# Kernel optimization log

Hardware: AMD Instinct MI355X
Metric: run time of the kernel (lower is better)

Reference implementation:

```python
import jax, jax.numpy as jnp
import numpy as np

B, S, T = 64, 48, 48
E, H = 512, 1024
V_SRC, V_TGT = 32000, 32000
PAD = 0


def setup_inputs() -> dict:
    key = jax.random.key(0)
    ks = jax.random.split(key, 24)
    def g(k, shape, scale=0.05):
        return jax.random.normal(k, shape, dtype=jnp.float32) * scale
    return {
        "src_ids": jax.random.randint(ks[0], (S, B), 0, V_SRC),
        "tgt_ids": jax.random.randint(ks[1], (T, B), 0, V_TGT),
        "src_lengths": S,
        "src_emb": g(ks[2], (V_SRC, E)).at[PAD].set(0.0),
        "tgt_emb": g(ks[3], (V_TGT, E)).at[PAD].set(0.0),
        "cnn_w": g(ks[4], (E, E, 2)),
        "cnn_b": g(ks[5], (E,)),
        "enc_Wih_f": g(ks[6], (4 * H, E)),
        "enc_Whh_f": g(ks[7], (4 * H, H)),
        "enc_bih_f": g(ks[8], (4 * H,)),
        "enc_bhh_f": g(ks[9], (4 * H,)),
        "enc_Wih_b": g(ks[10], (4 * H, E)),
        "enc_Whh_b": g(ks[11], (4 * H, H)),
        "enc_bih_b": g(ks[12], (4 * H,)),
        "enc_bhh_b": g(ks[13], (4 * H,)),
        "dec_Wih": g(ks[14], (4 * H, E + H)),
        "dec_Whh": g(ks[15], (4 * H, H)),
        "dec_bih": g(ks[16], (4 * H,)),
        "dec_bhh": g(ks[17], (4 * H,)),
        "Wh": g(ks[18], (H, 2 * H)),
        "Wc": g(ks[19], (H, 2 * H)),
        "Watt": g(ks[20], (H, 2 * H)),
        "Wcomb": g(ks[21], (H, 3 * H)),
        "Wvocab": g(ks[22], (V_TGT, H)),
    }


def _lstm_cell(x, h, c, Wih, Whh, bih, bhh):
    gates = x @ Wih.T + h @ Whh.T + bih + bhh  # (b, 4h)
    i, f, g, o = jnp.split(gates, 4, axis=-1)
    c_new = jax.nn.sigmoid(f) * c + jax.nn.sigmoid(i) * jnp.tanh(g)
    h_new = jax.nn.sigmoid(o) * jnp.tanh(c_new)
    return h_new, c_new


def _forward(src_ids, tgt_ids,
             src_emb, tgt_emb, cnn_w, cnn_b,
             enc_Wih_f, enc_Whh_f, enc_bih_f, enc_bhh_f,
             enc_Wih_b, enc_Whh_b, enc_bih_b, enc_bhh_b,
             dec_Wih, dec_Whh, dec_bih, dec_bhh,
             Wh, Wc, Watt, Wcomb, Wvocab):
    b = src_ids.shape[1]
    h = Wh.shape[0]
    # ---- encode ----
    X = src_emb[src_ids]                       # (S, b, E)
    Xc = jnp.transpose(X, (1, 2, 0))           # (b, E, S)
    # Conv1d kernel_size=2, padding='same' in torch pads (left=0, right=1)
    Xc = jax.lax.conv_general_dilated(Xc, cnn_w, window_strides=(1,),
                                      padding=[(0, 1)],
                                      dimension_numbers=("NCH", "OIH", "NCH"))
    Xc = Xc + cnn_b[None, :, None]
    X = jnp.transpose(Xc, (2, 0, 1))           # (S, b, E)

    h0 = jnp.zeros((b, h), dtype=X.dtype)
    def fstep(carry, x_t):
        hh, cc = carry
        hh, cc = _lstm_cell(x_t, hh, cc, enc_Wih_f, enc_Whh_f, enc_bih_f, enc_bhh_f)
        return (hh, cc), hh
    def bstep(carry, x_t):
        hh, cc = carry
        hh, cc = _lstm_cell(x_t, hh, cc, enc_Wih_b, enc_Whh_b, enc_bih_b, enc_bhh_b)
        return (hh, cc), hh
    (hf, cf), out_f = jax.lax.scan(fstep, (h0, h0), X)
    (hb, cb), out_b = jax.lax.scan(bstep, (h0, h0), X[::-1])
    out_b = out_b[::-1]
    enc_hiddens = jnp.concatenate([out_f, out_b], axis=-1)   # (S, b, 2h)
    enc_hiddens = jnp.transpose(enc_hiddens, (1, 0, 2))      # (b, S, 2h)
    dec_h = jnp.concatenate([hf, hb], axis=1) @ Wh.T         # (b, h)
    dec_c = jnp.concatenate([cf, cb], axis=1) @ Wc.T         # (b, h)

    # ---- decode ----
    enc_proj = enc_hiddens @ Watt.T            # (b, S, h)
    enc_mask = jnp.zeros((b, enc_hiddens.shape[1]), dtype=bool)  # all full length
    Y = tgt_emb[tgt_ids[:-1]]                  # (T-1, b, E)

    def dstep(carry, Y_t):
        hh, cc, o_prev = carry
        ybar = jnp.concatenate([o_prev, Y_t], axis=1)        # (b, h+E)
        hh, cc = _lstm_cell(ybar, hh, cc, dec_Wih, dec_Whh, dec_bih, dec_bhh)
        e_t = jnp.einsum("bh,bsh->bs", hh, enc_proj)
        e_t = jnp.where(enc_mask, -jnp.inf, e_t)
        alpha = jax.nn.softmax(e_t, axis=-1)
        a_t = jnp.einsum("bs,bsd->bd", alpha, enc_hiddens)   # (b, 2h)
        O_t = jnp.tanh(jnp.concatenate([a_t, hh], axis=1) @ Wcomb.T)  # dropout rate 0
        return (hh, cc, O_t), O_t

    o0 = jnp.zeros((b, h), dtype=X.dtype)
    _, combined = jax.lax.scan(dstep, (dec_h, dec_c, o0), Y)  # (T-1, b, h)

    P = jax.nn.log_softmax(combined @ Wvocab.T, axis=-1)      # (T-1, b, V)
    gold = tgt_ids[1:]                                        # (T-1, b)
    logp = jnp.take_along_axis(P, gold[..., None], axis=-1)[..., 0]
    tmask = (gold != PAD).astype(P.dtype)
    return (logp * tmask).sum(axis=0)                         # (b,)


def reference(src_ids, tgt_ids, src_lengths,
              src_emb, tgt_emb, cnn_w, cnn_b,
              enc_Wih_f, enc_Whh_f, enc_bih_f, enc_bhh_f,
              enc_Wih_b, enc_Whh_b, enc_bih_b, enc_bhh_b,
              dec_Wih, dec_Whh, dec_bih, dec_bhh,
              Wh, Wc, Watt, Wcomb, Wvocab):
    # src_lengths == S for every sentence (packed seq degenerates to full-length LSTM)
    return _forward(src_ids, tgt_ids, src_emb, tgt_emb, cnn_w, cnn_b,
                    enc_Wih_f, enc_Whh_f, enc_bih_f, enc_bhh_f,
                    enc_Wih_b, enc_Whh_b, enc_bih_b, enc_bhh_b,
                    dec_Wih, dec_Whh, dec_bih, dec_bhh,
                    Wh, Wc, Watt, Wcomb, Wvocab)
```

## Files before the change

kernel.cpp:

```cpp
#include <hip/hip_runtime.h>
#include <hip/hip_bf16.h>
#include <math.h>

using f32x4 = __attribute__((ext_vector_type(4))) float;
using s16x8 = __attribute__((ext_vector_type(8))) short;
typedef unsigned short u16;
typedef unsigned int u32;
typedef unsigned long long u64;

#define MFMA16(a,b,c) __builtin_amdgcn_mfma_f32_16x16x32_bf16(a,b,c,0,0,0)
#define SCOPE_A __HIP_MEMORY_SCOPE_AGENT
#define FP 16

__device__ __forceinline__ float bf2f(u16 u){
  union { u32 i; float f; } v; v.i = ((u32)u) << 16; return v.f;
}
__device__ __forceinline__ u16 f2bf(float f){
  union { float f; u32 i; } v; v.f = f;
  u32 x = v.i;
  return (u16)((x + 0x7fffu + ((x >> 16) & 1u)) >> 16);
}
__device__ __forceinline__ float sigm(float x){ return 1.0f/(1.0f + expf(-x)); }

__device__ __forceinline__ s16x8 pack8(const float* p){
  s16x8 r;
  #pragma unroll
  for (int i = 0; i < 8; ++i) r[i] = (short)f2bf(p[i]);
  return r;
}

__device__ __forceinline__ void coh_st32(void* p, u32 v){
  __hip_atomic_store((u32*)p, v, __ATOMIC_RELAXED, SCOPE_A);
}
__device__ __forceinline__ float u2f(u32 u){ union { u32 i; float f; } v; v.i = u; return v.f; }
__device__ __forceinline__ u32 f2u(float f){ union { float f; u32 i; } v; v.f = f; return v.i; }

__device__ __forceinline__ void poll(const int* flags, int n, int gen){
  for (int i = threadIdx.x; i < n; i += 256)
    while (__hip_atomic_load(flags + i*FP, __ATOMIC_RELAXED, SCOPE_A) < gen)
      __builtin_amdgcn_s_sleep(1);
  __syncthreads();
}
__device__ __forceinline__ void setflag(int* flag, int gen){
  __syncthreads();
  if (threadIdx.x == 0)
    __hip_atomic_store(flag, gen, __ATOMIC_RELAXED, SCOPE_A);
}

__device__ __forceinline__ void gemm_k1024(
    const u16* ap, const char* wb0, const char* wb1, int xo, int addb,
    f32x4& a0, f32x4& a1)
{
  #pragma unroll
  for (int c = 0; c < 2; ++c){
    s16x8 st[16];
    #pragma unroll
    for (int q = 0; q < 16; ++q) st[q] = *(const s16x8*)(ap + c*512 + q*32);
    #pragma unroll
    for (int q = 0; q < 16; ++q){
      int cb = (addb + (c*512 + q*32)*2) ^ xo;
      a0 = MFMA16(st[q], *(const s16x8*)(wb0 + cb), a0);
      a1 = MFMA16(st[q], *(const s16x8*)(wb1 + cb), a1);
    }
  }
}

__global__ void k_zero(float* __restrict__ p, long n){
  long i = (long)blockIdx.x*blockDim.x + threadIdx.x;
  long st = (long)gridDim.x*blockDim.x;
  for (; i < n; i += st) p[i] = 0.0f;
}

__global__ void k_cast_bf16(const float* __restrict__ src, u16* __restrict__ dst, long n){
  long i = ((long)blockIdx.x*blockDim.x + threadIdx.x)*4;
  long st = (long)gridDim.x*blockDim.x*4;
  for (; i < n; i += st){
    float4 v = *(const float4*)(src + i);
    *(ushort4*)(dst + i) = make_ushort4(f2bf(v.x), f2bf(v.y), f2bf(v.z), f2bf(v.w));
  }
}

__global__ void k_addv(const float* __restrict__ a, const float* __restrict__ b,
                       float* __restrict__ d, int n){
  int i = blockIdx.x*blockDim.x + threadIdx.x;
  if (i < n) d[i] = a[i] + b[i];
}

__global__ void k_repack_conv(const float* __restrict__ w, u16* __restrict__ dst){
  int i = blockIdx.x*256 + threadIdx.x;
  int o = i >> 9, ii = i & 511;
  dst[(size_t)o*1024 + ii]       = f2bf(w[((size_t)o*512 + ii)*2 + 0]);
  dst[(size_t)o*1024 + 512 + ii] = f2bf(w[((size_t)o*512 + ii)*2 + 1]);
}

__global__ void k_build_wy(const float* __restrict__ dWih, u16* __restrict__ Wy){
  int i = blockIdx.x*256 + threadIdx.x;
  int r = i >> 9, c = i & 511;
  Wy[(size_t)r*512 + c] = f2bf(dWih[(size_t)r*1536 + 1024 + c]);
}

__global__ void k_split_wcomb(const float* __restrict__ Wcomb,
                              u16* __restrict__ Wca, u16* __restrict__ Whp){
  int r = blockIdx.x;
  for (int c = threadIdx.x; c < 2048; c += 256)
    Wca[(size_t)r*2048 + c] = f2bf(Wcomb[(size_t)r*3072 + c]);
  for (int c = threadIdx.x; c < 1024; c += 256)
    Whp[(size_t)r*1024 + c] = f2bf(Wcomb[(size_t)r*3072 + 2048 + c]);
}

__global__ void k_gather_src(const int* __restrict__ ids, const float* __restrict__ emb,
                             u16* __restrict__ Aconv){
  int s = blockIdx.x;
  int b = blockIdx.y;
  int e = threadIdx.x*4;
  float4 v = make_float4(0.f,0.f,0.f,0.f);
  if (s < 48){ int id = ids[s*64 + b]; v = *(const float4*)(emb + (size_t)id*512 + e); }
  ushort4 u = make_ushort4(f2bf(v.x), f2bf(v.y), f2bf(v.z), f2bf(v.w));
  if (s < 48) *(ushort4*)(Aconv + ((size_t)(s*64 + b))*1024 + e) = u;
  if (s >= 1) *(ushort4*)(Aconv + ((size_t)((s-1)*64 + b))*1024 + 512 + e) = u;
}

__global__ void k_gather_y(const int* __restrict__ ids, const float* __restrict__ emb,
                           u16* __restrict__ Y){
  int t = blockIdx.x; int b = blockIdx.y; int e = threadIdx.x*4;
  int id = ids[t*64 + b];
  float4 v = *(const float4*)(emb + (size_t)id*512 + e);
  *(ushort4*)(Y + ((size_t)(t*64 + b))*512 + e) = make_ushort4(f2bf(v.x), f2bf(v.y), f2bf(v.z), f2bf(v.w));
}

template<bool OUT_BF16, bool PACKG>
__global__ __launch_bounds__(256) void k_gemm(
    const u16* __restrict__ A0, long lda0,
    const u16* __restrict__ A1, long lda1, int ksplit,
    const u16* __restrict__ W, int K,
    void* __restrict__ Out, long ldc,
    const float* __restrict__ bias)
{
  __shared__ __align__(16) u16 As[64][72];
  __shared__ __align__(16) u16 Ws[64][72];
  const int t = threadIdx.x;
  const int m0 = blockIdx.x*64, n0 = blockIdx.y*64;
  const int w = t >> 6, l = t & 63, lr = l & 15, lh = l >> 4;
  const int sr = t >> 2, sk = (t & 3) << 4;

  f32x4 acc[4] = {{0,0,0,0},{0,0,0,0},{0,0,0,0},{0,0,0,0}};

  for (int kc = 0; kc < K; kc += 64){
    {
      const u16* wp = W + (size_t)(n0 + sr)*K + kc + sk;
      *(s16x8*)&Ws[sr][sk]     = *(const s16x8*)wp;
      *(s16x8*)&Ws[sr][sk + 8] = *(const s16x8*)(wp + 8);
    }
    {
      const u16* ap = (kc < ksplit)
        ? A0 + (size_t)(m0 + sr)*lda0 + kc
        : A1 + (size_t)(m0 + sr)*lda1 + (kc - ksplit);
      ap += sk;
      *(s16x8*)&As[sr][sk]     = *(const s16x8*)ap;
      *(s16x8*)&As[sr][sk + 8] = *(const s16x8*)(ap + 8);
    }
    __syncthreads();
    #pragma unroll
    for (int kk = 0; kk < 64; kk += 32){
      s16x8 a = *(const s16x8*)&As[w*16 + lr][kk + lh*8];
      #pragma unroll
      for (int ct = 0; ct < 4; ++ct){
        s16x8 bfr = *(const s16x8*)&Ws[ct*16 + lr][kk + lh*8];
        acc[ct] = MFMA16(a, bfr, acc[ct]);
      }
    }
    __syncthreads();
  }
  #pragma unroll
  for (int ct = 0; ct < 4; ++ct){
    #pragma unroll
    for (int rr = 0; rr < 4; ++rr){
      long row = m0 + w*16 + lh*4 + rr;
      long col = n0 + ct*16 + lr;
      float v = acc[ct][rr];
      if (bias) v += bias[col];
      if (PACKG){
        long time = row >> 6, b = row & 63, g = col >> 10, j = col & 1023;
        ((u16*)Out)[((time*1024 + j)*4 + g)*64 + b] = f2bf(v);
      } else {
        long oi = row*ldc + col;
        if (OUT_BF16) ((u16*)Out)[oi] = f2bf(v);
        else          ((float*)Out)[oi] = v;
      }
    }
  }
}

__global__ __launch_bounds__(256) void k_enc_persist(
    const float* __restrict__ WhhF, const float* __restrict__ WhhB,
    const u16* __restrict__ GfP, const u16* __restrict__ GbP,
    u16* __restrict__ hEF, u16* __restrict__ hEB,
    const u16* __restrict__ hzero,
    float* __restrict__ cF, float* __restrict__ cB,
    u16* __restrict__ Aatt, u16* __restrict__ cfbf, u16* __restrict__ cbbf,
    int* Eflags)
{
  extern __shared__ char smem[];
  const int t = threadIdx.x, blk = blockIdx.x;
  const int dir = blk >> 6;
  const int j0 = (blk & 63) << 4;
  const float* Wsrc = dir ? WhhB : WhhF;
  const u16* GP = dir ? GbP : GfP;
  float* c = dir ? cB : cF;
  u16* cobf = dir ? cbbf : cfbf;
  u16* hE = dir ? hEB : hEF;

  for (int q = t; q < 64*128; q += 256){
    int row = q >> 7;
    int ck = (q & 127) << 3;
    int wrow = ((row >> 4)*1024) + j0 + (row & 15);
    s16x8 pk = pack8(Wsrc + (size_t)wrow*1024 + ck);
    *(s16x8*)(smem + row*2048 + ((ck*2) ^ ((row & 7) << 4))) = pk;
  }
  __syncthreads();

  const int w = t >> 6, l = t & 63, lr = l & 15, lh = l >> 4;
  const int lane_m = w*16 + lr;
  const int koff = lh*8;
  const char* wp0 = smem + lr*2048;
  const char* wp1 = smem + (16 + lr)*2048;
  const char* wp2 = smem + (32 + lr)*2048;
  const char* wp3 = smem + (48 + lr)*2048;
  const int xo = (lr & 7) << 4;
  const int j = j0 + lr;
  int* myflags = Eflags + dir*64*FP;
  const int myidx = blk & 63;

  for (int s = 0; s < 48; ++s){
    const u16* hin = s ? (hE + (size_t)(s - 1)*65536) : hzero;
    u16* hout      = hE + (size_t)s*65536;
    const int time = dir ? 47 - s : s;
    if (s) poll(myflags, 64, s);
    f32x4 a0 = {0,0,0,0}, a1 = {0,0,0,0}, a2 = {0,0,0,0}, a3 = {0,0,0,0};
    const u16* ap = hin + (size_t)lane_m*1024 + koff;
    #pragma unroll
    for (int cc = 0; cc < 2; ++cc){
      s16x8 st[16];
      #pragma unroll
      for (int q = 0; q < 16; ++q) st[q] = *(const s16x8*)(ap + cc*512 + q*32);
      #pragma unroll
      for (int q = 0; q < 16; ++q){
        int cb = ((cc*512 + q*32 + koff)*2) ^ xo;
        a0 = MFMA16(st[q], *(const s16x8*)(wp0 + cb), a0);
        a1 = MFMA16(st[q], *(const s16x8*)(wp1 + cb), a1);
        a2 = MFMA16(st[q], *(const s16x8*)(wp2 + cb), a2);
        a3 = MFMA16(st[q], *(const s16x8*)(wp3 + cb), a3);
      }
    }
    #pragma unroll
    for (int rr = 0; rr < 4; ++rr){
      int b = w*16 + lh*4 + rr;
      const u16* gp = GP + (((size_t)time*1024 + j)*4)*64 + b;
      float gi = a0[rr] + bf2f(gp[0]);
      float gf = a1[rr] + bf2f(gp[64]);
      float gg = a2[rr] + bf2f(gp[128]);
      float go = a3[rr] + bf2f(gp[192]);
      float cn = sigm(gf)*c[b*1024 + j] + sigm(gi)*tanhf(gg);
      float hn = sigm(go)*tanhf(cn);
      c[b*1024 + j] = cn;
      u16 hb = f2bf(hn);
      u32 hi2 = __shfl_down((u32)hb, 1);
      if ((lr & 1) == 0)
        coh_st32((u32*)hout + ((b*1024 + j) >> 1), (u32)hb | (hi2 << 16));
      Aatt[((size_t)b*48 + time)*2048 + dir*1024 + j] = hb;
      if (s == 47) cobf[b*1024 + j] = f2bf(cn);
    }
    setflag(myflags + myidx*FP, s + 1);
  }
}

__global__ __launch_bounds__(256) void k_dec_persist(
    const float* __restrict__ dWih, const float* __restrict__ dWhh,
    const u16* __restrict__ GyP,
    const u16* __restrict__ encP, const u16* __restrict__ encWc,
    const u16* __restrict__ Whp,
    const u16* __restrict__ hbinit, u16* __restrict__ hD,
    float* __restrict__ cdec,
    float* __restrict__ hp, u16* __restrict__ Cbf,
    const u16* __restrict__ obf_zero,
    int* Gflags, int* G2flags, int* Cflags)
{
  extern __shared__ char smem[];
  const int t = threadIdx.x, blk = blockIdx.x;
  const int w = t >> 6, l = t & 63, lr = l & 15, lh = l >> 4;
  const int lane_m = w*16 + lr;
  const int koff = lh*8;
  const int xo = (lr & 7) << 4;

  if (blk < 128){
    const int j0 = blk << 3;
    for (int q = t; q < 32*256; q += 256){
      int row = q >> 8;
      int ck = (q & 255) << 3;
      int wrow = ((row >> 3)*1024) + j0 + (row & 7);
      const float* src = (ck < 1024) ? dWih + (size_t)wrow*1536 + ck
                                     : dWhh + (size_t)wrow*1024 + (ck - 1024);
      s16x8 pk = pack8(src);
      *(s16x8*)(smem + row*4096 + ((ck*2) ^ ((row & 7) << 4))) = pk;
    }
    char* WhpL = smem + 131072;
    for (int q = t; q < 8*128; q += 256){
      int row = q >> 7, ck = (q & 127) << 3;
      s16x8 v = *(const s16x8*)(Whp + (size_t)(j0 + row)*1024 + ck);
      *(s16x8*)(WhpL + row*2048 + ((ck*2) ^ ((row & 7) << 4))) = v;
    }
    __syncthreads();
    const char* wp0 = smem + lr*4096;
    const char* wp1 = smem + (16 + lr)*4096;
    const char* wph = WhpL + (lr & 7)*2048;
    const int jj = lr & 7, gsel = lr >> 3;
    const int j = j0 + jj;

    s16x8 hreg[32];
    {
      const u16* ap = hbinit + (size_t)lane_m*1024 + koff;
      #pragma unroll
      for (int q = 0; q < 32; ++q) hreg[q] = *(const s16x8*)(ap + q*32);
    }

    for (int tt = 0; tt < 47; ++tt){
      u16* hout = hD + (size_t)tt*65536;
      f32x4 a0 = {0,0,0,0}, a1 = {0,0,0,0};
      #pragma unroll
      for (int q = 0; q < 32; ++q){
        int cb = ((1024 + q*32 + koff)*2) ^ xo;
        a0 = MFMA16(hreg[q], *(const s16x8*)(wp0 + cb), a0);
        a1 = MFMA16(hreg[q], *(const s16x8*)(wp1 + cb), a1);
      }
      if (tt) poll(Cflags, 64, tt);
      const u16* Ao = tt ? (Cbf + (size_t)(tt - 1)*65536) : obf_zero;
      gemm_k1024(Ao + (size_t)lane_m*1024 + koff, wp0, wp1, xo, koff*2, a0, a1);
      #pragma unroll
      for (int rr = 0; rr < 4; ++rr){
        float v0 = a0[rr], v1 = a1[rr];
        float p0 = __shfl_xor(v0, 8, 64);
        float p1 = __shfl_xor(v1, 8, 64);
        if (gsel == 0){
          int b = w*16 + lh*4 + rr;
          const u16* gp = GyP + (((size_t)tt*1024 + j)*4)*64 + b;
          float gi = v0 + bf2f(gp[0]);
          float gf = p0 + bf2f(gp[64]);
          float gg = v1 + bf2f(gp[128]);
          float go = p1 + bf2f(gp[192]);
          float cn = sigm(gf)*cdec[b*1024 + j] + sigm(gi)*tanhf(gg);
          float hn = sigm(go)*tanhf(cn);
          cdec[b*1024 + j] = cn;
          u16 hb = f2bf(hn);
          u32 hi2 = __shfl_down((u32)hb, 1);
          if ((jj & 1) == 0)
            coh_st32((u32*)hout + ((b*1024 + j) >> 1), (u32)hb | (hi2 << 16));
        }
      }
      setflag(Gflags + blk*FP, tt + 1);
      poll(Gflags, 128, tt + 1);
      {
        const u16* ap = hout + (size_t)lane_m*1024 + koff;
        #pragma unroll
        for (int q = 0; q < 32; ++q) hreg[q] = *(const s16x8*)(ap + q*32);
      }
      f32x4 hpacc = {0,0,0,0};
      #pragma unroll
      for (int q = 0; q < 32; ++q){
        int cb = ((q*32 + koff)*2) ^ xo;
        s16x8 bw = {0,0,0,0,0,0,0,0};
        if (lr < 8) bw = *(const s16x8*)(wph + cb);
        hpacc = MFMA16(hreg[q], bw, hpacc);
      }
      if (lr < 8){
        float* hpout = hp + (size_t)tt*65536;
        #pragma unroll
        for (int rr = 0; rr < 4; ++rr)
          coh_st32(&hpout[(size_t)(w*16 + lh*4 + rr)*1024 + j0 + lr], f2u(hpacc[rr]));
      }
      setflag(G2flags + blk*FP, tt + 1);
    }
  } else {
    const int b = blk - 128;
    u16* encPL = (u16*)smem;
    float* hs  = (float*)(smem + 98304);
    float* es  = (float*)(smem + 102400);
    float* al  = es + 48;
    float* sred= al + 48;
    for (int q = t; q < 48*128; q += 256){
      int row = q >> 7, ck = (q & 127) << 3;
      *(s16x8*)&encPL[row*1024 + ck] =
        *(const s16x8*)(encP + ((size_t)b*48 + row)*1024 + ck);
    }
    __syncthreads();

    for (int tt = 0; tt < 47; ++tt){
      poll(Gflags, 128, tt + 1);
      const u16* hrow = hD + (size_t)tt*65536 + (size_t)b*1024;
      {
        ushort4 v4 = ((const ushort4*)hrow)[t];
        hs[4*t]     = bf2f(v4.x);
        hs[4*t + 1] = bf2f(v4.y);
        hs[4*t + 2] = bf2f(v4.z);
        hs[4*t + 3] = bf2f(v4.w);
      }
      __syncthreads();
      for (int s2 = w; s2 < 48; s2 += 4){
        float p = 0.f;
        #pragma unroll
        for (int i = 0; i < 16; ++i)
          p += hs[l + 64*i]*bf2f(encPL[s2*1024 + l + 64*i]);
        #pragma unroll
        for (int d = 32; d >= 1; d >>= 1) p += __shfl_xor(p, d, 64);
        if (l == 0) es[s2] = p;
      }
      __syncthreads();
      if (t == 0){
        float m = es[0];
        for (int s2 = 1; s2 < 48; ++s2) m = fmaxf(m, es[s2]);
        float su = 0.f;
        for (int s2 = 0; s2 < 48; ++s2) su += expf(es[s2] - m);
        sred[0] = m; sred[1] = 1.0f/su;
      }
      __syncthreads();
      if (t < 48) al[t] = expf(es[t] - sred[0])*sred[1];
      __syncthreads();
      poll(G2flags, 128, tt + 1);
      int c0 = t*4;
      float4 hpv = *(const float4*)(hp + (size_t)tt*65536 + (size_t)b*1024 + c0);
      float acc0 = 0.f, acc1 = 0.f, acc2 = 0.f, acc3 = 0.f;
      const u16* ew = encWc + (size_t)b*48*1024 + c0;
      #pragma unroll 4
      for (int s2 = 0; s2 < 48; ++s2){
        float wgt = al[s2];
        ushort4 e4 = *(const ushort4*)(ew + (size_t)s2*1024);
        acc0 += wgt*bf2f(e4.x); acc1 += wgt*bf2f(e4.y);
        acc2 += wgt*bf2f(e4.z); acc3 += wgt*bf2f(e4.w);
      }
      float v0 = tanhf(hpv.x + acc0), v1 = tanhf(hpv.y + acc1);
      float v2 = tanhf(hpv.z + acc2), v3 = tanhf(hpv.w + acc3);
      size_t oi = (size_t)tt*65536 + (size_t)b*1024 + c0;
      coh_st32((u32*)Cbf + (oi >> 1),     (u32)f2bf(v0) | ((u32)f2bf(v1) << 16));
      coh_st32((u32*)Cbf + (oi >> 1) + 1, (u32)f2bf(v2) | ((u32)f2bf(v3) << 16));
      setflag(Cflags + b*FP, tt + 1);
    }
  }
}

#define VNS 25
__global__ __launch_bounds__(256) void k_vocab_lse(
    const u16* __restrict__ Cbf, const u16* __restrict__ Wv, float2* __restrict__ partials)
{
  __shared__ __align__(16) u16 As[128][72];
  __shared__ __align__(16) u16 Bs[128][72];
  __shared__ float2 mg[128][2];
  int rb = blockIdx.x, sp = blockIdx.y;
  int m0 = rb*128;
  int t = threadIdx.x, w = t >> 6, l = t & 63, lr = l & 15, lh = l >> 4;
  int wr = w >> 1, wc = w & 1;
  int sr = t >> 1, sk = (t & 1) << 5;

  float mrun[4][4], srun[4][4];
  #pragma unroll
  for (int m = 0; m < 4; ++m)
    #pragma unroll
    for (int rr = 0; rr < 4; ++rr){ mrun[m][rr] = -INFINITY; srun[m][rr] = 0.f; }

  for (int nt = 0; nt < 10; ++nt){
    int n0 = sp*1280 + nt*128;
    f32x4 acc[4][4];
    #pragma unroll
    for (int m = 0; m < 4; ++m)
      #pragma unroll
      for (int n = 0; n < 4; ++n) acc[m][n] = (f32x4){0,0,0,0};

    for (int kc = 0; kc < 1024; kc += 64){
      int ar = m0 + sr; if (ar > 3007) ar = 3007;
      const u16* ap = Cbf + (size_t)ar*1024 + kc + sk;
      const u16* wp = Wv + (size_t)(n0 + sr)*1024 + kc + sk;
      #pragma unroll
      for (int q = 0; q < 4; ++q){
        *(s16x8*)&As[sr][sk + q*8] = *(const s16x8*)(ap + q*8);
        *(s16x8*)&Bs[sr][sk + q*8] = *(const s16x8*)(wp + q*8);
      }
      __syncthreads();
      #pragma unroll
      for (int kk = 0; kk < 64; kk += 32){
        s16x8 af[4], bf[4];
        #pragma unroll
        for (int m = 0; m < 4; ++m)
          af[m] = *(const s16x8*)&As[wr*64 + m*16 + lr][kk + lh*8];
        #pragma unroll
        for (int n = 0; n < 4; ++n)
          bf[n] = *(const s16x8*)&Bs[wc*64 + n*16 + lr][kk + lh*8];
        #pragma unroll
        for (int m = 0; m < 4; ++m)
          #pragma unroll
          for (int n = 0; n < 4; ++n)
            acc[m][n] = MFMA16(af[m], bf[n], acc[m][n]);
      }
      __syncthreads();
    }
    #pragma unroll
    for (int m = 0; m < 4; ++m){
      #pragma unroll
      for (int rr = 0; rr < 4; ++rr){
        float tm = fmaxf(fmaxf(acc[m][0][rr], acc[m][1][rr]),
                         fmaxf(acc[m][2][rr], acc[m][3][rr]));
        #pragma unroll
        for (int d = 1; d < 16; d <<= 1) tm = fmaxf(tm, __shfl_xor(tm, d, 64));
        float ts = expf(acc[m][0][rr] - tm) + expf(acc[m][1][rr] - tm)
                 + expf(acc[m][2][rr] - tm) + expf(acc[m][3][rr] - tm);
        #pragma unroll
        for (int d = 1; d < 16; d <<= 1) ts += __shfl_xor(ts, d, 64);
        if (tm > mrun[m][rr]){ srun[m][rr] = srun[m][rr]*expf(mrun[m][rr] - tm) + ts; mrun[m][rr] = tm; }
        else srun[m][rr] += ts*expf(tm - mrun[m][rr]);
      }
    }
  }
  __syncthreads();
  if (lr == 0){
    #pragma unroll
    for (int m = 0; m < 4; ++m)
      #pragma unroll
      for (int rr = 0; rr < 4; ++rr)
        mg[wr*64 + m*16 + lh*4 + rr][wc] = make_float2(mrun[m][rr], srun[m][rr]);
  }
  __syncthreads();
  if (t < 128){
    float2 p0 = mg[t][0], p1 = mg[t][1];
    float m = fmaxf(p0.x, p1.x);
    float s = p0.y*expf(p0.x - m) + p1.y*expf(p1.x - m);
    long row = m0 + t;
    if (row < 3008) partials[row*VNS + sp] = make_float2(m, s);
  }
}

__global__ void k_lse(const float2* __restrict__ partials, float* __restrict__ lse){
  int r = blockIdx.x*256 + threadIdx.x;
  if (r >= 3008) return;
  float m = -INFINITY, s = 0.f;
  for (int i = 0; i < VNS; ++i){
    float2 p = partials[r*VNS + i];
    if (p.x > m){ s = s*expf(m - p.x) + p.y; m = p.x; }
    else s += p.y*expf(p.x - m);
  }
  lse[r] = m + logf(s);
}

__global__ __launch_bounds__(256) void k_gold(const u16* __restrict__ Cbf,
                                              const u16* __restrict__ Wv,
                                              const int* __restrict__ tgt,
                                              float* __restrict__ gold){
  int w = threadIdx.x >> 6, l = threadIdx.x & 63;
  int r = blockIdx.x*4 + w;
  int tt = r >> 6, b = r & 63;
  int gid = tgt[(tt + 1)*64 + b];
  const u16* cp = Cbf + (size_t)r*1024;
  const u16* wp = Wv + (size_t)gid*1024;
  float p = 0.f;
  for (int i = l; i < 1024; i += 64) p += bf2f(cp[i])*bf2f(wp[i]);
  for (int d = 32; d >= 1; d >>= 1) p += __shfl_xor(p, d, 64);
  if (l == 0) gold[r] = p;
}

__global__ void k_final(const float* __restrict__ gold, const float* __restrict__ lse,
                        const int* __restrict__ tgt, float* __restrict__ out){
  int b = threadIdx.x;
  if (b >= 64) return;
  float acc = 0.f;
  for (int t = 0; t < 47; ++t){
    int gid = tgt[(t + 1)*64 + b];
    if (gid != 0) acc += gold[t*64 + b] - lse[t*64 + b];
  }
  out[b] = acc;
}

extern "C" void kernel_launch(void* const* d_in, const int* in_sizes, int n_in,
                              void* d_out, int out_size, void* d_ws, size_t ws_size,
                              hipStream_t stream)
{
  (void)in_sizes; (void)n_in; (void)out_size; (void)ws_size;
  const int*   src_ids = (const int*)d_in[0];
  const int*   tgt_ids = (const int*)d_in[1];
  const float* src_emb = (const float*)d_in[3];
  const float* tgt_emb = (const float*)d_in[4];
  const float* cnn_w   = (const float*)d_in[5];
  const float* cnn_b   = (const float*)d_in[6];
  const float* eWih_f  = (const float*)d_in[7];
  const float* eWhh_f  = (const float*)d_in[8];
  const float* ebih_f  = (const float*)d_in[9];
  const float* ebhh_f  = (const float*)d_in[10];
  const float* eWih_b  = (const float*)d_in[11];
  const float* eWhh_b  = (const float*)d_in[12];
  const float* ebih_b  = (const float*)d_in[13];
  const float* ebhh_b  = (const float*)d_in[14];
  const float* dWih    = (const float*)d_in[15];
  const float* dWhh    = (const float*)d_in[16];
  const float* dbih    = (const float*)d_in[17];
  const float* dbhh    = (const float*)d_in[18];
  const float* Wh      = (const float*)d_in[19];
  const float* Wc      = (const float*)d_in[20];
  const float* Watt    = (const float*)d_in[21];
  const float* Wcomb   = (const float*)d_in[22];
  const float* Wvocab  = (const float*)d_in[23];

  char* ws = (char*)d_ws;
  size_t off = 0;
  auto alloc = [&](size_t bytes)->char*{
    char* p = ws + off;
    off = (off + bytes + 255) & ~(size_t)255;
    return p;
  };

  float* cF     = (float*)alloc((size_t)65536*4);
  float* cB     = (float*)alloc((size_t)65536*4);
  u16* obf_zero = (u16*)alloc((size_t)65536*2);
  int* bar      = (int*)alloc(40960);
  size_t zero_floats = ((size_t)262144*2 + 131072 + 40960)/4;
  int* Eflags  = bar;
  int* Gflags  = bar + 2048;
  int* G2flags = bar + 4096;
  int* Cflags  = bar + 6144;

  u16* Wconv_bf = (u16*)alloc((size_t)512*1024*2);
  u16* Wih_f_bf = (u16*)alloc((size_t)4096*512*2);
  u16* Wih_b_bf = (u16*)alloc((size_t)4096*512*2);
  u16* Wy_bf    = (u16*)alloc((size_t)4096*512*2);
  u16* Wh_bf    = (u16*)alloc((size_t)1024*2048*2);
  u16* Wc_bf    = (u16*)alloc((size_t)1024*2048*2);
  u16* Watt_bf  = (u16*)alloc((size_t)1024*2048*2);
  u16* Wca_bf   = (u16*)alloc((size_t)1024*2048*2);
  u16* Whp_bf   = (u16*)alloc((size_t)1024*1024*2);
  u16* Wv_bf    = (u16*)alloc((size_t)32000*1024*2);
  float* benc_f = (float*)alloc(4096*4);
  float* benc_b = (float*)alloc(4096*4);
  float* bdec   = (float*)alloc(4096*4);

  u16* Aconv    = (u16*)alloc((size_t)3072*1024*2);
  u16* Xc       = (u16*)alloc((size_t)3072*512*2);
  u16* GfP      = (u16*)alloc((size_t)48*1024*256*2);
  u16* GbP      = (u16*)alloc((size_t)48*1024*256*2);
  u16* GyP      = (u16*)alloc((size_t)47*1024*256*2);
  u16* Ybf      = (u16*)alloc((size_t)3008*512*2);
  u16* Aatt     = (u16*)alloc((size_t)3072*2048*2);
  u16* encP     = (u16*)alloc((size_t)3072*1024*2);
  u16* encWc    = (u16*)alloc((size_t)3072*1024*2);
  u16* hEF      = (u16*)alloc((size_t)48*65536*2);
  u16* hEB      = (u16*)alloc((size_t)48*65536*2);
  u16* cfbf     = (u16*)alloc((size_t)65536*2);
  u16* cbbf     = (u16*)alloc((size_t)65536*2);
  u16* hbinit   = (u16*)alloc((size_t)65536*2);
  u16* hD       = (u16*)alloc((size_t)47*65536*2);
  float* cdec   = (float*)alloc((size_t)65536*4);
  float* hp     = (float*)alloc((size_t)47*65536*4);
  u16* Cbf      = (u16*)alloc((size_t)3008*1024*2);
  float2* partials=(float2*)alloc((size_t)3008*VNS*8);
  float* lse    = (float*)alloc(3008*4);
  float* gold   = (float*)alloc(3008*4);

  k_zero<<<256, 256, 0, stream>>>(cF, (long)zero_floats);

  auto cgrid = [](long n)->int{ long g = (n/4 + 255)/256; return (int)(g > 1024 ? 1024 : g); };
  k_cast_bf16<<<cgrid(4096*512), 256, 0, stream>>>(eWih_f, Wih_f_bf, (long)4096*512);
  k_cast_bf16<<<cgrid(4096*512), 256, 0, stream>>>(eWih_b, Wih_b_bf, (long)4096*512);
  k_cast_bf16<<<cgrid(1024*2048), 256, 0, stream>>>(Wh, Wh_bf, (long)1024*2048);
  k_cast_bf16<<<cgrid(1024*2048), 256, 0, stream>>>(Wc, Wc_bf, (long)1024*2048);
  k_cast_bf16<<<cgrid(1024*2048), 256, 0, stream>>>(Watt, Watt_bf, (long)1024*2048);
  k_cast_bf16<<<cgrid((long)32000*1024), 256, 0, stream>>>(Wvocab, Wv_bf, (long)32000*1024);

  k_addv<<<16, 256, 0, stream>>>(ebih_f, ebhh_f, benc_f, 4096);
  k_addv<<<16, 256, 0, stream>>>(ebih_b, ebhh_b, benc_b, 4096);
  k_addv<<<16, 256, 0, stream>>>(dbih, dbhh, bdec, 4096);

  k_repack_conv<<<1024, 256, 0, stream>>>(cnn_w, Wconv_bf);
  k_build_wy<<<8192, 256, 0, stream>>>(dWih, Wy_bf);
  k_split_wcomb<<<1024, 256, 0, stream>>>(Wcomb, Wca_bf, Whp_bf);

  k_gather_src<<<dim3(49, 64), 128, 0, stream>>>(src_ids, src_emb, Aconv);
  k_gather_y<<<dim3(47, 64), 128, 0, stream>>>(tgt_ids, tgt_emb, Ybf);

  k_gemm<true, false><<<dim3(48, 8), 256, 0, stream>>>(
      Aconv, 1024, Aconv, 1024, 1024, Wconv_bf, 1024, Xc, 512, cnn_b);
  k_gemm<true, true><<<dim3(48, 64), 256, 0, stream>>>(
      Xc, 512, Xc, 512, 512, Wih_f_bf, 512, GfP, 0, benc_f);
  k_gemm<true, true><<<dim3(48, 64), 256, 0, stream>>>(
      Xc, 512, Xc, 512, 512, Wih_b_bf, 512, GbP, 0, benc_b);
  k_gemm<true, true><<<dim3(47, 64), 256, 0, stream>>>(
      Ybf, 512, Ybf, 512, 512, Wy_bf, 512, GyP, 0, bdec);

  k_enc_persist<<<128, 256, 131072, stream>>>(
      eWhh_f, eWhh_b, GfP, GbP, hEF, hEB, obf_zero, cF, cB,
      Aatt, cfbf, cbbf, Eflags);

  k_gemm<true, false><<<dim3(1, 16), 256, 0, stream>>>(
      hEF + (size_t)47*65536, 1024, hEB + (size_t)47*65536, 1024, 1024,
      Wh_bf, 2048, hbinit, 1024, nullptr);
  k_gemm<false, false><<<dim3(1, 16), 256, 0, stream>>>(
      cfbf, 1024, cbbf, 1024, 1024, Wc_bf, 2048, cdec, 1024, nullptr);
  k_gemm<true, false><<<dim3(48, 16), 256, 0, stream>>>(
      Aatt, 2048, Aatt, 2048, 2048, Watt_bf, 2048, encP, 1024, nullptr);
  k_gemm<true, false><<<dim3(48, 16), 256, 0, stream>>>(
      Aatt, 2048, Aatt, 2048, 2048, Wca_bf, 2048, encWc, 1024, nullptr);

  k_dec_persist<<<192, 256, 147456, stream>>>(
      dWih, dWhh, GyP, encP, encWc, Whp_bf, hbinit, hD, cdec,
      hp, Cbf, obf_zero, Gflags, G2flags, Cflags);

  k_vocab_lse<<<dim3(24, VNS), 256, 0, stream>>>(Cbf, Wv_bf, partials);
  k_lse<<<12, 256, 0, stream>>>(partials, lse);
  k_gold<<<752, 256, 0, stream>>>(Cbf, Wv_bf, tgt_ids, gold);
  k_final<<<1, 64, 0, stream>>>(gold, lse, tgt_ids, (float*)d_out);
}
```

Baseline: 2.585 ms.

## Overlap decoder input GEMM and vocab cast with encoder recurrence; pack flags

Measured after the change: 2.769 ms. 1.07x slower.

```diff
diff --git a/kernel.cpp b/kernel.cpp
--- a/kernel.cpp
+++ b/kernel.cpp
@@ -10,7 +10,6 @@
 
 #define MFMA16(a,b,c) __builtin_amdgcn_mfma_f32_16x16x32_bf16(a,b,c,0,0,0)
 #define SCOPE_A __HIP_MEMORY_SCOPE_AGENT
-#define FP 16
 
 __device__ __forceinline__ float bf2f(u16 u){
   union { u32 i; float f; } v; v.i = ((u32)u) << 16; return v.f;
@@ -37,7 +36,7 @@
 
 __device__ __forceinline__ void poll(const int* flags, int n, int gen){
   for (int i = threadIdx.x; i < n; i += 256)
-    while (__hip_atomic_load(flags + i*FP, __ATOMIC_RELAXED, SCOPE_A) < gen)
+    while (__hip_atomic_load(flags + i, __ATOMIC_RELAXED, SCOPE_A) < gen)
       __builtin_amdgcn_s_sleep(1);
   __syncthreads();
 }
@@ -198,10 +197,61 @@
     const u16* __restrict__ hzero,
     float* __restrict__ cF, float* __restrict__ cB,
     u16* __restrict__ Aatt, u16* __restrict__ cfbf, u16* __restrict__ cbbf,
-    int* Eflags)
+    int* Eflags,
+    const u16* __restrict__ Ybf, const u16* __restrict__ WyBf,
+    const float* __restrict__ bdec, u16* __restrict__ GyP,
+    const float* __restrict__ Wv, u16* __restrict__ WvBf)
 {
   extern __shared__ char smem[];
   const int t = threadIdx.x, blk = blockIdx.x;
+  const int w = t >> 6, l = t & 63, lr = l & 15, lh = l >> 4;
+
+  if (blk >= 128){
+    const int hb = blk - 128;
+    u16 (*As)[72] = (u16(*)[72])smem;
+    u16 (*Ws)[72] = (u16(*)[72])(smem + 64*72*2);
+    const int sr = t >> 2, sk = (t & 3) << 4;
+    for (int tile = hb; tile < 47*64; tile += 128){
+      int m0 = (tile % 47)*64, n0 = (tile / 47)*64;
+      f32x4 acc[4] = {{0,0,0,0},{0,0,0,0},{0,0,0,0},{0,0,0,0}};
+      for (int kc = 0; kc < 512; kc += 64){
+        const u16* wp = WyBf + (size_t)(n0 + sr)*512 + kc + sk;
+        *(s16x8*)&Ws[sr][sk]     = *(const s16x8*)wp;
+        *(s16x8*)&Ws[sr][sk + 8] = *(const s16x8*)(wp + 8);
+        const u16* ap = Ybf + (size_t)(m0 + sr)*512 + kc + sk;
+        *(s16x8*)&As[sr][sk]     = *(const s16x8*)ap;
+        *(s16x8*)&As[sr][sk + 8] = *(const s16x8*)(ap + 8);
+        __syncthreads();
+        #pragma unroll
+        for (int kk = 0; kk < 64; kk += 32){
+          s16x8 a = *(const s16x8*)&As[w*16 + lr][kk + lh*8];
+          #pragma unroll
+          for (int ct = 0; ct < 4; ++ct){
+            s16x8 bfr = *(const s16x8*)&Ws[ct*16 + lr][kk + lh*8];
+            acc[ct] = MFMA16(a, bfr, acc[ct]);
+          }
+        }
+        __syncthreads();
+      }
+      #pragma unroll
+      for (int ct = 0; ct < 4; ++ct){
+        #pragma unroll
+        for (int rr = 0; rr < 4; ++rr){
+          long row = m0 + w*16 + lh*4 + rr;
+          long col = n0 + ct*16 + lr;
+          float v = acc[ct][rr] + bdec[col];
+          long time = row >> 6, b = row & 63, g = col >> 10, j = col & 1023;
+          GyP[((time*1024 + j)*4 + g)*64 + b] = f2bf(v);
+        }
+      }
+    }
+    for (long i = ((long)hb*256 + t)*4; i < (long)32000*1024; i += (long)128*256*4){
+      float4 v = *(const float4*)(Wv + i);
+      *(ushort4*)(WvBf + i) = make_ushort4(f2bf(v.x), f2bf(v.y), f2bf(v.z), f2bf(v.w));
+    }
+    return;
+  }
+
   const int dir = blk >> 6;
   const int j0 = (blk & 63) << 4;
   const float* Wsrc = dir ? WhhB : WhhF;
@@ -209,6 +259,8 @@
   float* c = dir ? cB : cF;
   u16* cobf = dir ? cbbf : cfbf;
   u16* hE = dir ? hEB : hEF;
+  int* myflags = Eflags + dir*64;
+  const int myidx = blk & 63;
 
   for (int q = t; q < 64*128; q += 256){
     int row = q >> 7;
@@ -219,7 +271,6 @@
   }
   __syncthreads();
 
-  const int w = t >> 6, l = t & 63, lr = l & 15, lh = l >> 4;
   const int lane_m = w*16 + lr;
   const int koff = lh*8;
   const char* wp0 = smem + lr*2048;
@@ -228,8 +279,6 @@
   const char* wp3 = smem + (48 + lr)*2048;
   const int xo = (lr & 7) << 4;
   const int j = j0 + lr;
-  int* myflags = Eflags + dir*64*FP;
-  const int myidx = blk & 63;
 
   for (int s = 0; s < 48; ++s){
     const u16* hin = s ? (hE + (size_t)(s - 1)*65536) : hzero;
@@ -270,7 +319,7 @@
       Aatt[((size_t)b*48 + time)*2048 + dir*1024 + j] = hb;
       if (s == 47) cobf[b*1024 + j] = f2bf(cn);
     }
-    setflag(myflags + myidx*FP, s + 1);
+    setflag(myflags + myidx, s + 1);
   }
 }
 
@@ -356,7 +405,7 @@
             coh_st32((u32*)hout + ((b*1024 + j) >> 1), (u32)hb | (hi2 << 16));
         }
       }
-      setflag(Gflags + blk*FP, tt + 1);
+      setflag(Gflags + blk, tt + 1);
       poll(Gflags, 128, tt + 1);
       {
         const u16* ap = hout + (size_t)lane_m*1024 + koff;
@@ -377,7 +426,7 @@
         for (int rr = 0; rr < 4; ++rr)
           coh_st32(&hpout[(size_t)(w*16 + lh*4 + rr)*1024 + j0 + lr], f2u(hpacc[rr]));
       }
-      setflag(G2flags + blk*FP, tt + 1);
+      setflag(G2flags + blk, tt + 1);
     }
   } else {
     const int b = blk - 128;
@@ -441,7 +490,7 @@
       size_t oi = (size_t)tt*65536 + (size_t)b*1024 + c0;
       coh_st32((u32*)Cbf + (oi >> 1),     (u32)f2bf(v0) | ((u32)f2bf(v1) << 16));
       coh_st32((u32*)Cbf + (oi >> 1) + 1, (u32)f2bf(v2) | ((u32)f2bf(v3) << 16));
-      setflag(Cflags + b*FP, tt + 1);
+      setflag(Cflags + b, tt + 1);
     }
   }
 }
@@ -615,12 +664,12 @@
   float* cF     = (float*)alloc((size_t)65536*4);
   float* cB     = (float*)alloc((size_t)65536*4);
   u16* obf_zero = (u16*)alloc((size_t)65536*2);
-  int* bar      = (int*)alloc(40960);
-  size_t zero_floats = ((size_t)262144*2 + 131072 + 40960)/4;
+  int* bar      = (int*)alloc(4096);
+  size_t zero_floats = ((size_t)262144*2 + 131072 + 4096)/4;
   int* Eflags  = bar;
-  int* Gflags  = bar + 2048;
-  int* G2flags = bar + 4096;
-  int* Cflags  = bar + 6144;
+  int* Gflags  = bar + 128;
+  int* G2flags = bar + 256;
+  int* Cflags  = bar + 384;
 
   u16* Wconv_bf = (u16*)alloc((size_t)512*1024*2);
   u16* Wih_f_bf = (u16*)alloc((size_t)4096*512*2);
@@ -666,7 +715,6 @@
   k_cast_bf16<<<cgrid(1024*2048), 256, 0, stream>>>(Wh, Wh_bf, (long)1024*2048);
   k_cast_bf16<<<cgrid(1024*2048), 256, 0, stream>>>(Wc, Wc_bf, (long)1024*2048);
   k_cast_bf16<<<cgrid(1024*2048), 256, 0, stream>>>(Watt, Watt_bf, (long)1024*2048);
-  k_cast_bf16<<<cgrid((long)32000*1024), 256, 0, stream>>>(Wvocab, Wv_bf, (long)32000*1024);
 
   k_addv<<<16, 256, 0, stream>>>(ebih_f, ebhh_f, benc_f, 4096);
   k_addv<<<16, 256, 0, stream>>>(ebih_b, ebhh_b, benc_b, 4096);
@@ -685,12 +733,11 @@
       Xc, 512, Xc, 512, 512, Wih_f_bf, 512, GfP, 0, benc_f);
   k_gemm<true, true><<<dim3(48, 64), 256, 0, stream>>>(
       Xc, 512, Xc, 512, 512, Wih_b_bf, 512, GbP, 0, benc_b);
-  k_gemm<true, true><<<dim3(47, 64), 256, 0, stream>>>(
-      Ybf, 512, Ybf, 512, 512, Wy_bf, 512, GyP, 0, bdec);
-
-  k_enc_persist<<<128, 256, 131072, stream>>>(
+
+  k_enc_persist<<<256, 256, 131072, stream>>>(
       eWhh_f, eWhh_b, GfP, GbP, hEF, hEB, obf_zero, cF, cB,
-      Aatt, cfbf, cbbf, Eflags);
+      Aatt, cfbf, cbbf, Eflags,
+      Ybf, Wy_bf, bdec, GyP, Wvocab, Wv_bf);
 
   k_gemm<true, false><<<dim3(1, 16), 256, 0, stream>>>(
       hEF + (size_t)47*65536, 1024, hEB + (size_t)47*65536, 1024, 1024,
```
